# Kernel optimization log

Measured on AMD Instinct MI355X. Metric: run time of the kernel, lower is better.

## Reference

```python
import jax, jax.numpy as jnp
import numpy as np

N_NODES = 50000
N_EDGES = 800000
IN_FEATS = 256
HIDDEN = 128
HEADS = 2
NEG_SLOPE = 0.2


def gat_conv(x, edge_index, W, att_src, att_dst, bias, heads, out_c, concat):
    """PyG-style GATConv: linear -> per-edge attention logits -> segment
    softmax over destination neighborhoods -> scatter-add aggregate.
    Self-loops are added (PyG default add_self_loops=True)."""
    N = x.shape[0]
    h = (x @ W.T).reshape(N, heads, out_c)           # [N,H,C]
    loop = jnp.arange(N)
    src = jnp.concatenate([edge_index[0], loop])      # [E+N]
    dst = jnp.concatenate([edge_index[1], loop])
    a_src = jnp.sum(h * att_src, axis=-1)             # [N,H]
    a_dst = jnp.sum(h * att_dst, axis=-1)
    alpha = a_src[src] + a_dst[dst]                   # [E+N,H]
    alpha = jax.nn.leaky_relu(alpha, NEG_SLOPE)
    amax = jax.ops.segment_max(alpha, dst, num_segments=N)
    alpha = jnp.exp(alpha - amax[dst])
    denom = jax.ops.segment_sum(alpha, dst, num_segments=N)
    alpha = alpha / denom[dst]
    msg = h[src] * alpha[..., None]                   # [E+N,H,C]
    out = jax.ops.segment_sum(msg, dst, num_segments=N)  # [N,H,C]
    if concat:
        out = out.reshape(N, heads * out_c)
    else:
        out = out.mean(axis=1)
    return out + bias


def setup_inputs() -> dict:
    key = jax.random.key(0)
    ks = jax.random.split(key, 12)
    x = jax.random.normal(ks[0], (N_NODES, IN_FEATS), dtype=jnp.float32)
    edge_index = jax.random.randint(ks[1], (2, N_EDGES), 0, N_NODES, dtype=jnp.int64)
    s = 0.1
    W1 = jax.random.normal(ks[2], (HEADS * HIDDEN, IN_FEATS), dtype=jnp.float32) * s
    att_src1 = jax.random.normal(ks[3], (1, HEADS, HIDDEN), dtype=jnp.float32) * s
    att_dst1 = jax.random.normal(ks[4], (1, HEADS, HIDDEN), dtype=jnp.float32) * s
    b1 = jnp.zeros((HEADS * HIDDEN,), dtype=jnp.float32)
    W2 = jax.random.normal(ks[5], (HIDDEN, HEADS * HIDDEN), dtype=jnp.float32) * s
    att_src2 = jax.random.normal(ks[6], (1, 1, HIDDEN), dtype=jnp.float32) * s
    att_dst2 = jax.random.normal(ks[7], (1, 1, HIDDEN), dtype=jnp.float32) * s
    b2 = jnp.zeros((HIDDEN,), dtype=jnp.float32)
    return {"x": x, "edge_index": edge_index,
            "W1": W1, "att_src1": att_src1, "att_dst1": att_dst1, "b1": b1,
            "W2": W2, "att_src2": att_src2, "att_dst2": att_dst2, "b2": b2}


def reference(x, edge_index, W1, att_src1, att_dst1, b1, W2, att_src2, att_dst2, b2):
    h = gat_conv(x, edge_index, W1, att_src1, att_dst1, b1, HEADS, HIDDEN, True)
    h = jax.nn.relu(h)
    out = gat_conv(h, edge_index, W2, att_src2, att_dst2, b2, 1, HIDDEN, False)
    return out
```

## Files before the change

### kernel.cpp

```cpp
#include <hip/hip_runtime.h>
#include <hip/hip_bf16.h>


typedef _Float16 half8v __attribute__((ext_vector_type(8)));
typedef _Float16 half4v __attribute__((ext_vector_type(4)));
typedef _Float16 half2v __attribute__((ext_vector_type(2)));
typedef float f32x4 __attribute__((ext_vector_type(4)));


template <typename TA>
__global__ __launch_bounds__(256) void gemm_mfma_kernel(
    const TA* __restrict__ A,
    const float* __restrict__ B,
    _Float16* __restrict__ C,
    int M, int N, int K)
{
    constexpr int BM = 128, BK = 32, LDA = 40;
    __shared__ _Float16 Ah[BM * LDA];
    __shared__ _Float16 Bh[BM * LDA];

    const int tid = threadIdx.x;
    const int m0 = blockIdx.x * BM;
    const int n0 = blockIdx.y * BM;
    const int w  = tid >> 6;
    const int l  = tid & 63;
    const int wm = (w >> 1) * 64;
    const int wn = (w & 1) * 64;
    const int lr = l & 15;
    const int lq = l >> 4;

    f32x4 acc[4][4] = {};

    for (int k0 = 0; k0 < K; k0 += BK) {
        if constexpr (__is_same(TA, float)) {
#pragma unroll
            for (int it = 0; it < 4; ++it) {
                const int row = (tid >> 3) + it * 32;
                const int gm  = min(m0 + row, M - 1);
                const int c4  = (tid & 7) * 4;
                float4 v = *reinterpret_cast<const float4*>(A + (long)gm * K + k0 + c4);
                half4v o = { (_Float16)v.x, (_Float16)v.y, (_Float16)v.z, (_Float16)v.w };
                *reinterpret_cast<half4v*>(&Ah[row * LDA + c4]) = o;
            }
        } else {
#pragma unroll
            for (int it = 0; it < 2; ++it) {
                const int row = (tid >> 2) + it * 64;
                const int gm  = min(m0 + row, M - 1);
                const int c8  = (tid & 3) * 8;
                float4 v = *reinterpret_cast<const float4*>((const char*)A + ((long)gm * K + k0 + c8) * 2);
                *reinterpret_cast<float4*>(&Ah[row * LDA + c8]) = v;
            }
        }
#pragma unroll
        for (int it = 0; it < 4; ++it) {
            const int row = (tid >> 3) + it * 32;
            const int c4  = (tid & 7) * 4;
            float4 v = *reinterpret_cast<const float4*>(B + (long)(n0 + row) * K + k0 + c4);
            half4v o = { (_Float16)v.x, (_Float16)v.y, (_Float16)v.z, (_Float16)v.w };
            *reinterpret_cast<half4v*>(&Bh[row * LDA + c4]) = o;
        }
        __syncthreads();

        half8v af[4], bf[4];
#pragma unroll
        for (int i = 0; i < 4; ++i)
            af[i] = *reinterpret_cast<const half8v*>(&Ah[(wm + i * 16 + lr) * LDA + lq * 8]);
#pragma unroll
        for (int j = 0; j < 4; ++j)
            bf[j] = *reinterpret_cast<const half8v*>(&Bh[(wn + j * 16 + lr) * LDA + lq * 8]);
#pragma unroll
        for (int i = 0; i < 4; ++i)
#pragma unroll
            for (int j = 0; j < 4; ++j)
                acc[i][j] = __builtin_amdgcn_mfma_f32_16x16x32_f16(af[i], bf[j], acc[i][j], 0, 0, 0);
        __syncthreads();
    }

#pragma unroll
    for (int i = 0; i < 4; ++i) {
        const int gm_base = m0 + wm + i * 16 + lq * 4;
#pragma unroll
        for (int r = 0; r < 4; ++r) {
            const int gm = gm_base + r;
            if (gm < M) {
#pragma unroll
                for (int j = 0; j < 4; ++j) {
                    const int gn = n0 + wn + j * 16 + lr;
                    C[(long)gm * N + gn] = (_Float16)acc[i][j][r];
                }
            }
        }
    }
}


__global__ void count_kernel(const int* __restrict__ dst, int* __restrict__ deg, int E)
{
    const int e = blockIdx.x * blockDim.x + threadIdx.x;
    if (e < E) atomicAdd(&deg[dst[e]], 1);
}

__global__ __launch_bounds__(256) void block_scan_kernel(
    const int* __restrict__ deg, int* __restrict__ pre, int* __restrict__ blk, int n)
{
    __shared__ int s[256];
    const int t = threadIdx.x;
    const int base = blockIdx.x * 1024 + t * 4;
    int4 d = make_int4(-1, -1, -1, -1);
    if (base + 3 < n) d = *reinterpret_cast<const int4*>(deg + base);
    else {
        if (base + 0 < n) d.x = deg[base + 0];
        if (base + 1 < n) d.y = deg[base + 1];
        if (base + 2 < n) d.z = deg[base + 2];
        if (base + 3 < n) d.w = deg[base + 3];
    }
    const int v0 = d.x + 1, v1 = d.y + 1, v2 = d.z + 1, v3 = d.w + 1;
    s[t] = v0 + v1 + v2 + v3;
    __syncthreads();
#pragma unroll
    for (int o = 1; o < 256; o <<= 1) {
        int val = 0;
        if (t >= o) val = s[t - o];
        __syncthreads();
        s[t] += val;
        __syncthreads();
    }
    int run = (t == 0) ? 0 : s[t - 1];
    int4 o4;
    o4.x = run; run += v0;
    o4.y = run; run += v1;
    o4.z = run; run += v2;
    o4.w = run; run += v3;
    if (base + 3 < n) *reinterpret_cast<int4*>(pre + base) = o4;
    else {
        if (base + 0 < n) pre[base + 0] = o4.x;
        if (base + 1 < n) pre[base + 1] = o4.y;
        if (base + 2 < n) pre[base + 2] = o4.z;
        if (base + 3 < n) pre[base + 3] = o4.w;
    }
    if (t == 255) blk[blockIdx.x] = s[255];
}

__global__ void total_scan_kernel(const int* __restrict__ blk, int* __restrict__ blk_off,
                                  int* __restrict__ off_end, int nb)
{
    const int l = threadIdx.x;
    const int self = (l < nb) ? blk[l] : 0;
    int v = self;
#pragma unroll
    for (int o = 1; o < 64; o <<= 1) {
        int u = __shfl_up(v, o, 64);
        if (l >= o) v += u;
    }
    if (l < nb) blk_off[l] = v - self;
    if (l == nb - 1) *off_end = v;
}

__global__ __launch_bounds__(256) void finalize_scan_kernel(
    const int* __restrict__ pre, const int* __restrict__ blk_off,
    int* __restrict__ off, int* __restrict__ cursor, int n)
{
    const int t = threadIdx.x;
    const int base = blockIdx.x * 1024 + t * 4;
    const int add = blk_off[blockIdx.x];
    if (base + 3 < n) {
        int4 p = *reinterpret_cast<const int4*>(pre + base);
        p.x += add; p.y += add; p.z += add; p.w += add;
        *reinterpret_cast<int4*>(off + base) = p;
        *reinterpret_cast<int4*>(cursor + base) = p;
    } else {
#pragma unroll
        for (int k = 0; k < 4; ++k)
            if (base + k < n) {
                const int v = pre[base + k] + add;
                off[base + k] = v;
                cursor[base + k] = v;
            }
    }
}

__global__ void scatter_kernel(const int* __restrict__ src, const int* __restrict__ dst,
                               int* __restrict__ cursor, int* __restrict__ csr_src,
                               int E, int N)
{
    const int e = blockIdx.x * blockDim.x + threadIdx.x;
    if (e < E) {
        const int d = dst[e];
        const int p = atomicAdd(&cursor[d], 1);
        csr_src[p] = src[e];
    } else if (e < E + N) {
        const int nn = e - E;
        const int p = atomicAdd(&cursor[nn], 1);
        csr_src[p] = nn;
    }
}


template <int H>
__global__ __launch_bounds__(256) void att_kernel(
    const _Float16* __restrict__ h,
    const float* __restrict__ att_s,
    const float* __restrict__ att_d,
    float* __restrict__ a_s,
    float* __restrict__ a_d,
    int N)
{
    const int g = (blockIdx.x * 256 + threadIdx.x) >> 6;
    const int l = threadIdx.x & 63;
    if (g >= N * H) return;
    const int n  = g / H;
    const int hh = g % H;
    const _Float16* row = h + (long)n * (H * 128) + hh * 128;
    const float* asv = att_s + hh * 128;
    const float* adv = att_d + hh * 128;
    const float v0 = (float)row[l], v1 = (float)row[l + 64];
    float ss = v0 * asv[l] + v1 * asv[l + 64];
    float dd = v0 * adv[l] + v1 * adv[l + 64];
#pragma unroll
    for (int o = 32; o > 0; o >>= 1) {
        ss += __shfl_xor(ss, o, 64);
        dd += __shfl_xor(dd, o, 64);
    }
    if (l == 0) { a_s[g] = ss; a_d[g] = dd; }
}


#define AGG_TILE 64

template <int H, int C, int VPT, bool RELU, typename TOUT>
__global__ __launch_bounds__(H * C / VPT) void aggregate_kernel(
    const int* __restrict__ csr_off,
    const int* __restrict__ csr_src,
    const _Float16* __restrict__ h,
    const float* __restrict__ a_s,
    const float* __restrict__ a_d,
    const float* __restrict__ bias,
    TOUT* __restrict__ out)
{
    const int d   = blockIdx.x;
    const int t   = threadIdx.x;
    const int col = t * VPT;
    const int hh  = col / C;

    __shared__ int   s_src[AGG_TILE];
    __shared__ float s_w[AGG_TILE][H];

    const int beg = csr_off[d];
    const int end = csr_off[d + 1];

    float acc[VPT] = {};
    float wsum = 0.f;

    for (int base = beg; base < end; base += AGG_TILE) {
        const int len = min(AGG_TILE, end - base);
        if (t < len) {
            const int s = csr_src[base + t];
            s_src[t] = s;
#pragma unroll
            for (int h2 = 0; h2 < H; ++h2) {
                float logit = a_s[s * H + h2] + a_d[d * H + h2];
                logit = logit > 0.f ? logit : 0.2f * logit;
                s_w[t][h2] = __expf(logit);
            }
        }
        __syncthreads();
#pragma unroll 4
        for (int j = 0; j < len; ++j) {
            const float w = s_w[j][hh];
            const int   s = s_src[j];
            if constexpr (VPT == 4) {
                half4v hv = *reinterpret_cast<const half4v*>(h + (long)s * (H * C) + col);
                acc[0] += w * (float)hv.x;
                acc[1] += w * (float)hv.y;
                acc[2] += w * (float)hv.z;
                acc[3] += w * (float)hv.w;
            } else {
                half2v hv = *reinterpret_cast<const half2v*>(h + (long)s * (H * C) + col);
                acc[0] += w * (float)hv.x;
                acc[1] += w * (float)hv.y;
            }
            wsum += w;
        }
        __syncthreads();
    }

    const float inv = 1.f / wsum;
    float r[VPT];
#pragma unroll
    for (int k = 0; k < VPT; ++k) {
        r[k] = acc[k] * inv + bias[col + k];
        if (RELU) r[k] = r[k] > 0.f ? r[k] : 0.f;
    }
    if constexpr (__is_same(TOUT, _Float16)) {
#pragma unroll
        for (int k = 0; k < VPT; ++k)
            out[(long)d * (H * C) + col + k] = (_Float16)r[k];
    } else {
#pragma unroll
        for (int k = 0; k < VPT; ++k)
            out[(long)d * (H * C) + col + k] = r[k];
    }
}


extern "C" void kernel_launch(void* const* d_in, const int* in_sizes, int n_in,
                              void* d_out, int out_size, void* d_ws, size_t ws_size,
                              hipStream_t stream)
{
    const float* x    = (const float*)d_in[0];
    const int*   eidx = (const int*)d_in[1];
    const float* W1   = (const float*)d_in[2];
    const float* as1  = (const float*)d_in[3];
    const float* ad1  = (const float*)d_in[4];
    const float* b1   = (const float*)d_in[5];
    const float* W2   = (const float*)d_in[6];
    const float* as2  = (const float*)d_in[7];
    const float* ad2  = (const float*)d_in[8];
    const float* b2   = (const float*)d_in[9];
    float* out = (float*)d_out;

    const int IN_FEATS = 256;
    const int N = in_sizes[0] / IN_FEATS;
    const int E = in_sizes[1] / 2;

    const int* esrc = eidx;
    const int* edst = eidx + E;

    size_t off = 0;
    auto alloc = [&](size_t bytes) -> void* {
        void* p = (char*)d_ws + off;
        off += (bytes + 255) & ~(size_t)255;
        return p;
    };
    _Float16* h1h   = (_Float16*)alloc((size_t)N * 256 * 2);
    _Float16* o1h   = (_Float16*)alloc((size_t)N * 256 * 2);
    _Float16* h2h   = (_Float16*)alloc((size_t)N * 128 * 2);
    float* a1s      = (float*)alloc((size_t)N * 2 * 4);
    float* a1d      = (float*)alloc((size_t)N * 2 * 4);
    float* a2s      = (float*)alloc((size_t)N * 4);
    float* a2d      = (float*)alloc((size_t)N * 4);
    int*   deg      = (int*)alloc((size_t)N * 4);
    int*   pre      = (int*)alloc((size_t)N * 4);
    int*   cursor   = (int*)alloc((size_t)N * 4);
    int*   csr_off  = (int*)alloc((size_t)(N + 1) * 4);
    int*   csr_src  = (int*)alloc((size_t)(E + N) * 4);
    int*   blk      = (int*)alloc(64 * 4);
    int*   blk_off  = (int*)alloc(64 * 4);

    const int nbScan = (N + 1023) / 1024;

    hipMemsetAsync(deg, 0, (size_t)N * 4, stream);
    count_kernel<<<(E + 255) / 256, 256, 0, stream>>>(edst, deg, E);
    block_scan_kernel<<<nbScan, 256, 0, stream>>>(deg, pre, blk, N);
    total_scan_kernel<<<1, 64, 0, stream>>>(blk, blk_off, csr_off + N, nbScan);
    finalize_scan_kernel<<<nbScan, 256, 0, stream>>>(pre, blk_off, csr_off, cursor, N);
    scatter_kernel<<<(E + N + 255) / 256, 256, 0, stream>>>(esrc, edst, cursor, csr_src, E, N);

    {
        dim3 grid((N + 127) / 128, 256 / 128);
        gemm_mfma_kernel<float><<<grid, 256, 0, stream>>>(x, W1, h1h, N, 256, 256);
    }
    att_kernel<2><<<(N * 2 + 3) / 4, 256, 0, stream>>>(h1h, as1, ad1, a1s, a1d, N);
    aggregate_kernel<2, 128, 4, true, _Float16><<<N, 64, 0, stream>>>(
        csr_off, csr_src, h1h, a1s, a1d, b1, o1h);

    {
        dim3 grid((N + 127) / 128, 128 / 128);
        gemm_mfma_kernel<_Float16><<<grid, 256, 0, stream>>>(o1h, W2, h2h, N, 128, 256);
    }
    att_kernel<1><<<(N + 3) / 4, 256, 0, stream>>>(h2h, as2, ad2, a2s, a2d, N);
    aggregate_kernel<1, 128, 2, false, float><<<N, 64, 0, stream>>>(
        csr_off, csr_src, h2h, a2s, a2d, b2, out);
}
```

Measured before the change: 359.2 us.

## Pack four nodes per aggregate block, widen GEMM1 tile, vectorize CSR build

```diff
diff --git a/kernel.cpp b/kernel.cpp
--- a/kernel.cpp
+++ b/kernel.cpp
@@ -8,20 +8,90 @@
 typedef float f32x4 __attribute__((ext_vector_type(4)));
 
 
-template <typename TA>
-__global__ __launch_bounds__(256) void gemm_mfma_kernel(
-    const TA* __restrict__ A,
+__global__ __launch_bounds__(512) void gemm1_kernel(
+    const float* __restrict__ A,
     const float* __restrict__ B,
     _Float16* __restrict__ C,
     int M, int N, int K)
 {
+    constexpr int BM = 128, BN = 256, BK = 32, LDA = 40;
+    __shared__ _Float16 Ah[BM * LDA];
+    __shared__ _Float16 Bh[BN * LDA];
+
+    const int tid = threadIdx.x;
+    const int m0 = blockIdx.x * BM;
+    const int w  = tid >> 6;
+    const int l  = tid & 63;
+    const int wm = (w >> 2) * 64;
+    const int wn = (w & 3) * 64;
+    const int lr = l & 15;
+    const int lq = l >> 4;
+
+    f32x4 acc[4][4] = {};
+
+    for (int k0 = 0; k0 < K; k0 += BK) {
+#pragma unroll
+        for (int it = 0; it < 2; ++it) {
+            const int row = (tid >> 3) + it * 64;
+            const int gm  = min(m0 + row, M - 1);
+            const int c4  = (tid & 7) * 4;
+            float4 v = *reinterpret_cast<const float4*>(A + (long)gm * K + k0 + c4);
+            half4v o = { (_Float16)v.x, (_Float16)v.y, (_Float16)v.z, (_Float16)v.w };
+            *reinterpret_cast<half4v*>(&Ah[row * LDA + c4]) = o;
+        }
+#pragma unroll
+        for (int it = 0; it < 4; ++it) {
+            const int row = (tid >> 3) + it * 64;
+            const int c4  = (tid & 7) * 4;
+            float4 v = *reinterpret_cast<const float4*>(B + (long)row * K + k0 + c4);
+            half4v o = { (_Float16)v.x, (_Float16)v.y, (_Float16)v.z, (_Float16)v.w };
+            *reinterpret_cast<half4v*>(&Bh[row * LDA + c4]) = o;
+        }
+        __syncthreads();
+
+        half8v af[4], bf[4];
+#pragma unroll
+        for (int i = 0; i < 4; ++i)
+            af[i] = *reinterpret_cast<const half8v*>(&Ah[(wm + i * 16 + lr) * LDA + lq * 8]);
+#pragma unroll
+        for (int j = 0; j < 4; ++j)
+            bf[j] = *reinterpret_cast<const half8v*>(&Bh[(wn + j * 16 + lr) * LDA + lq * 8]);
+#pragma unroll
+        for (int i = 0; i < 4; ++i)
+#pragma unroll
+            for (int j = 0; j < 4; ++j)
+                acc[i][j] = __builtin_amdgcn_mfma_f32_16x16x32_f16(af[i], bf[j], acc[i][j], 0, 0, 0);
+        __syncthreads();
+    }
+
+#pragma unroll
+    for (int i = 0; i < 4; ++i) {
+        const int gm_base = m0 + wm + i * 16 + lq * 4;
+#pragma unroll
+        for (int r = 0; r < 4; ++r) {
+            const int gm = gm_base + r;
+            if (gm < M) {
+#pragma unroll
+                for (int j = 0; j < 4; ++j)
+                    C[(long)gm * N + wn + j * 16 + lr] = (_Float16)acc[i][j][r];
+            }
+        }
+    }
+}
+
+
+__global__ __launch_bounds__(256) void gemm2_kernel(
+    const _Float16* __restrict__ A,
+    const float* __restrict__ B,
+    _Float16* __restrict__ C,
+    int M, int N, int K)
+{
     constexpr int BM = 128, BK = 32, LDA = 40;
     __shared__ _Float16 Ah[BM * LDA];
     __shared__ _Float16 Bh[BM * LDA];
 
     const int tid = threadIdx.x;
     const int m0 = blockIdx.x * BM;
-    const int n0 = blockIdx.y * BM;
     const int w  = tid >> 6;
     const int l  = tid & 63;
     const int wm = (w >> 1) * 64;
@@ -32,31 +102,19 @@
     f32x4 acc[4][4] = {};
 
     for (int k0 = 0; k0 < K; k0 += BK) {
-        if constexpr (__is_same(TA, float)) {
-#pragma unroll
-            for (int it = 0; it < 4; ++it) {
-                const int row = (tid >> 3) + it * 32;
-                const int gm  = min(m0 + row, M - 1);
-                const int c4  = (tid & 7) * 4;
-                float4 v = *reinterpret_cast<const float4*>(A + (long)gm * K + k0 + c4);
-                half4v o = { (_Float16)v.x, (_Float16)v.y, (_Float16)v.z, (_Float16)v.w };
-                *reinterpret_cast<half4v*>(&Ah[row * LDA + c4]) = o;
-            }
-        } else {
-#pragma unroll
-            for (int it = 0; it < 2; ++it) {
-                const int row = (tid >> 2) + it * 64;
-                const int gm  = min(m0 + row, M - 1);
-                const int c8  = (tid & 3) * 8;
-                float4 v = *reinterpret_cast<const float4*>((const char*)A + ((long)gm * K + k0 + c8) * 2);
-                *reinterpret_cast<float4*>(&Ah[row * LDA + c8]) = v;
-            }
+#pragma unroll
+        for (int it = 0; it < 2; ++it) {
+            const int row = (tid >> 2) + it * 64;
+            const int gm  = min(m0 + row, M - 1);
+            const int c8  = (tid & 3) * 8;
+            float4 v = *reinterpret_cast<const float4*>((const char*)A + ((long)gm * K + k0 + c8) * 2);
+            *reinterpret_cast<float4*>(&Ah[row * LDA + c8]) = v;
         }
 #pragma unroll
         for (int it = 0; it < 4; ++it) {
             const int row = (tid >> 3) + it * 32;
             const int c4  = (tid & 7) * 4;
-            float4 v = *reinterpret_cast<const float4*>(B + (long)(n0 + row) * K + k0 + c4);
+            float4 v = *reinterpret_cast<const float4*>(B + (long)row * K + k0 + c4);
             half4v o = { (_Float16)v.x, (_Float16)v.y, (_Float16)v.z, (_Float16)v.w };
             *reinterpret_cast<half4v*>(&Bh[row * LDA + c4]) = o;
         }
@@ -85,10 +143,8 @@
             const int gm = gm_base + r;
             if (gm < M) {
 #pragma unroll
-                for (int j = 0; j < 4; ++j) {
-                    const int gn = n0 + wn + j * 16 + lr;
-                    C[(long)gm * N + gn] = (_Float16)acc[i][j][r];
-                }
+                for (int j = 0; j < 4; ++j)
+                    C[(long)gm * N + wn + j * 16 + lr] = (_Float16)acc[i][j][r];
             }
         }
     }
@@ -97,8 +153,16 @@
 
 __global__ void count_kernel(const int* __restrict__ dst, int* __restrict__ deg, int E)
 {
-    const int e = blockIdx.x * blockDim.x + threadIdx.x;
-    if (e < E) atomicAdd(&deg[dst[e]], 1);
+    const int e4 = (blockIdx.x * blockDim.x + threadIdx.x) * 4;
+    if (e4 + 3 < E) {
+        const int4 d = *reinterpret_cast<const int4*>(dst + e4);
+        atomicAdd(&deg[d.x], 1);
+        atomicAdd(&deg[d.y], 1);
+        atomicAdd(&deg[d.z], 1);
+        atomicAdd(&deg[d.w], 1);
+    } else {
+        for (int k = e4; k < E; ++k) atomicAdd(&deg[dst[k]], 1);
+    }
 }
 
 __global__ __launch_bounds__(256) void block_scan_kernel(
@@ -184,16 +248,25 @@
                                int* __restrict__ cursor, int* __restrict__ csr_src,
                                int E, int N)
 {
-    const int e = blockIdx.x * blockDim.x + threadIdx.x;
-    if (e < E) {
-        const int d = dst[e];
-        const int p = atomicAdd(&cursor[d], 1);
-        csr_src[p] = src[e];
-    } else if (e < E + N) {
-        const int nn = e - E;
-        const int p = atomicAdd(&cursor[nn], 1);
-        csr_src[p] = nn;
-    }
+    const int e4 = (blockIdx.x * blockDim.x + threadIdx.x) * 4;
+    if (e4 + 3 < E) {
+        const int4 s = *reinterpret_cast<const int4*>(src + e4);
+        const int4 d = *reinterpret_cast<const int4*>(dst + e4);
+        csr_src[atomicAdd(&cursor[d.x], 1)] = s.x;
+        csr_src[atomicAdd(&cursor[d.y], 1)] = s.y;
+        csr_src[atomicAdd(&cursor[d.z], 1)] = s.z;
+        csr_src[atomicAdd(&cursor[d.w], 1)] = s.w;
+    } else if (e4 < E) {
+        for (int k = e4; k < E; ++k)
+            csr_src[atomicAdd(&cursor[dst[k]], 1)] = src[k];
+    } else {
+        const int nn = (e4 - E) / 4 * 4 + (0);
+    }
+    const int tid = blockIdx.x * blockDim.x + threadIdx.x;
+    const int eBlocks = (E + 3) / 4;
+    const int nn = tid - eBlocks;
+    if (nn >= 0 && nn < N)
+        csr_src[atomicAdd(&cursor[nn], 1)] = nn;
 }
 
 
@@ -226,80 +299,95 @@
 }
 
 
-#define AGG_TILE 64
-
 template <int H, int C, int VPT, bool RELU, typename TOUT>
-__global__ __launch_bounds__(H * C / VPT) void aggregate_kernel(
+__global__ __launch_bounds__(256) void aggregate_kernel(
     const int* __restrict__ csr_off,
     const int* __restrict__ csr_src,
     const _Float16* __restrict__ h,
     const float* __restrict__ a_s,
     const float* __restrict__ a_d,
     const float* __restrict__ bias,
-    TOUT* __restrict__ out)
-{
-    const int d   = blockIdx.x;
-    const int t   = threadIdx.x;
-    const int col = t * VPT;
-    const int hh  = col / C;
-
-    __shared__ int   s_src[AGG_TILE];
-    __shared__ float s_w[AGG_TILE][H];
+    TOUT* __restrict__ out,
+    int N)
+{
+    const int wave = threadIdx.x >> 6;
+    const int l    = threadIdx.x & 63;
+    const int col  = l * VPT;
+    const int hh   = col / C;
+    const int d    = blockIdx.x * 4 + wave;
+
+    __shared__ float s_w[4][64][H];
+
+    if (d >= N) return;
 
     const int beg = csr_off[d];
     const int end = csr_off[d + 1];
 
+    float ad_loc[H];
+#pragma unroll
+    for (int h2 = 0; h2 < H; ++h2) ad_loc[h2] = a_d[d * H + h2];
+
     float acc[VPT] = {};
     float wsum = 0.f;
 
-    for (int base = beg; base < end; base += AGG_TILE) {
-        const int len = min(AGG_TILE, end - base);
-        if (t < len) {
-            const int s = csr_src[base + t];
-            s_src[t] = s;
+    for (int base = beg; base < end; base += 64) {
+        const int len = min(64, end - base);
+        int s = 0;
+        if (l < len) {
+            s = csr_src[base + l];
 #pragma unroll
             for (int h2 = 0; h2 < H; ++h2) {
-                float logit = a_s[s * H + h2] + a_d[d * H + h2];
+                float logit = a_s[s * H + h2] + ad_loc[h2];
                 logit = logit > 0.f ? logit : 0.2f * logit;
-                s_w[t][h2] = __expf(logit);
+                s_w[wave][l][h2] = __expf(logit);
             }
         }
-        __syncthreads();
 #pragma unroll 4
         for (int j = 0; j < len; ++j) {
-            const float w = s_w[j][hh];
-            const int   s = s_src[j];
+            const int   sj = __shfl(s, j, 64);
+            const float w  = s_w[wave][j][hh];
             if constexpr (VPT == 4) {
-                half4v hv = *reinterpret_cast<const half4v*>(h + (long)s * (H * C) + col);
+                half4v hv = *reinterpret_cast<const half4v*>(h + (long)sj * (H * C) + col);
                 acc[0] += w * (float)hv.x;
                 acc[1] += w * (float)hv.y;
                 acc[2] += w * (float)hv.z;
                 acc[3] += w * (float)hv.w;
             } else {
-                half2v hv = *reinterpret_cast<const half2v*>(h + (long)s * (H * C) + col);
+                half2v hv = *reinterpret_cast<const half2v*>(h + (long)sj * (H * C) + col);
                 acc[0] += w * (float)hv.x;
                 acc[1] += w * (float)hv.y;
             }
             wsum += w;
         }
-        __syncthreads();
     }
 
     const float inv = 1.f / wsum;
-    float r[VPT];
-#pragma unroll
-    for (int k = 0; k < VPT; ++k) {
-        r[k] = acc[k] * inv + bias[col + k];
-        if (RELU) r[k] = r[k] > 0.f ? r[k] : 0.f;
-    }
     if constexpr (__is_same(TOUT, _Float16)) {
-#pragma unroll
-        for (int k = 0; k < VPT; ++k)
-            out[(long)d * (H * C) + col + k] = (_Float16)r[k];
+        _Float16 o[VPT];
+#pragma unroll
+        for (int k = 0; k < VPT; ++k) {
+            float r = acc[k] * inv + bias[col + k];
+            if (RELU) r = r > 0.f ? r : 0.f;
+            o[k] = (_Float16)r;
+        }
+        if constexpr (VPT == 4)
+            *reinterpret_cast<half4v*>(out + (long)d * (H * C) + col) =
+                half4v{o[0], o[1], o[2], o[3]};
+        else
+            *reinterpret_cast<half2v*>(out + (long)d * (H * C) + col) =
+                half2v{o[0], o[1]};
     } else {
-#pragma unroll
-        for (int k = 0; k < VPT; ++k)
-            out[(long)d * (H * C) + col + k] = r[k];
+        float r[VPT];
+#pragma unroll
+        for (int k = 0; k < VPT; ++k) {
+            r[k] = acc[k] * inv + bias[col + k];
+            if (RELU) r[k] = r[k] > 0.f ? r[k] : 0.f;
+        }
+        if constexpr (VPT == 2)
+            *reinterpret_cast<float2*>(out + (long)d * (H * C) + col) = make_float2(r[0], r[1]);
+        else
+#pragma unroll
+            for (int k = 0; k < VPT; ++k) out[(long)d * (H * C) + col + k] = r[k];
     }
 }
 
@@ -351,25 +439,23 @@
     const int nbScan = (N + 1023) / 1024;
 
     hipMemsetAsync(deg, 0, (size_t)N * 4, stream);
-    count_kernel<<<(E + 255) / 256, 256, 0, stream>>>(edst, deg, E);
+    count_kernel<<<(E / 4 + 255) / 256, 256, 0, stream>>>(edst, deg, E);
     block_scan_kernel<<<nbScan, 256, 0, stream>>>(deg, pre, blk, N);
     total_scan_kernel<<<1, 64, 0, stream>>>(blk, blk_off, csr_off + N, nbScan);
     finalize_scan_kernel<<<nbScan, 256, 0, stream>>>(pre, blk_off, csr_off, cursor, N);
-    scatter_kernel<<<(E + N + 255) / 256, 256, 0, stream>>>(esrc, edst, cursor, csr_src, E, N);
-
     {
-        dim3 grid((N + 127) / 128, 256 / 128);
-        gemm_mfma_kernel<float><<<grid, 256, 0, stream>>>(x, W1, h1h, N, 256, 256);
-    }
+        const int eThreads = (E + 3) / 4 + N;
+        scatter_kernel<<<(eThreads + 255) / 256, 256, 0, stream>>>(
+            esrc, edst, cursor, csr_src, E, N);
+    }
+
+    gemm1_kernel<<<(N + 127) / 128, 512, 0, stream>>>(x, W1, h1h, N, 256, 256);
     att_kernel<2><<<(N * 2 + 3) / 4, 256, 0, stream>>>(h1h, as1, ad1, a1s, a1d, N);
-    aggregate_kernel<2, 128, 4, true, _Float16><<<N, 64, 0, stream>>>(
-        csr_off, csr_src, h1h, a1s, a1d, b1, o1h);
-
-    {
-        dim3 grid((N + 127) / 128, 128 / 128);
-        gemm_mfma_kernel<_Float16><<<grid, 256, 0, stream>>>(o1h, W2, h2h, N, 128, 256);
-    }
+    aggregate_kernel<2, 128, 4, true, _Float16><<<(N + 3) / 4, 256, 0, stream>>>(
+        csr_off, csr_src, h1h, a1s, a1d, b1, o1h, N);
+
+    gemm2_kernel<<<(N + 127) / 128, 256, 0, stream>>>(o1h, W2, h2h, N, 128, 256);
     att_kernel<1><<<(N + 3) / 4, 256, 0, stream>>>(h2h, as2, ad2, a2s, a2d, N);
-    aggregate_kernel<1, 128, 2, false, float><<<N, 64, 0, stream>>>(
-        csr_off, csr_src, h2h, a2s, a2d, b2, out);
-}
+    aggregate_kernel<1, 128, 2, false, float><<<(N + 3) / 4, 256, 0, stream>>>(
+        csr_off, csr_src, h2h, a2s, a2d, b2, out, N);
+}
```

Result: slower. 381.6 us (+6.3%).
